# Performance work log

Measured on AMD Instinct MI355X. Metric: run time of the kernel, lower is better.

## Reference

```python
import jax, jax.numpy as jnp
import numpy as np

D_MODEL = 1024
N_HEADS = 16
ADAPTIVE_TEMP = 1.0
LN_EPS = 1e-5


def _sinusoidal_pe(max_len, d_model):
    pos = np.arange(max_len)[:, None].astype(np.float32)
    div = np.exp(np.arange(0, d_model, 2).astype(np.float32) * (-np.log(10000.0) / d_model))
    pe = np.zeros((max_len, d_model), dtype=np.float32)
    pe[:, 0::2] = np.sin(pos * div)
    pe[:, 1::2] = np.cos(pos * div)
    return jnp.asarray(pe)


def _mlp2(q, w1, b1, w2, b2):
    # Linear(1,h) -> ReLU -> Linear(h,d)
    return jax.nn.relu(q @ w1 + b1) @ w2 + b2


def setup_inputs() -> dict:
    key = jax.random.key(0)
    ks = jax.random.split(key, 24)
    B, T, D = 2, 2048, D_MODEL
    H2 = D // 2
    s = 0.02
    inp = {
        "x": jax.random.normal(ks[0], (B, T, D), jnp.float32),
        "quantile": jax.random.uniform(ks[1], (B, 1), jnp.float32),
        "quantile_importance": jax.random.uniform(ks[2], (100,), jnp.float32),
        "Wq": jax.random.normal(ks[3], (D, D), jnp.float32) * s,
        "bq": jnp.zeros((D,), jnp.float32),
        "Wk": jax.random.normal(ks[4], (D, D), jnp.float32) * s,
        "bk": jnp.zeros((D,), jnp.float32),
        "Wv": jax.random.normal(ks[5], (D, D), jnp.float32) * s,
        "bv": jnp.zeros((D,), jnp.float32),
        "Wo": jax.random.normal(ks[6], (D, D), jnp.float32) * s,
        "bo": jnp.zeros((D,), jnp.float32),
        "qpq_w1": jax.random.normal(ks[7], (1, H2), jnp.float32) * s,
        "qpq_b1": jnp.zeros((H2,), jnp.float32),
        "qpq_w2": jax.random.normal(ks[8], (H2, D), jnp.float32) * s,
        "qpq_b2": jnp.zeros((D,), jnp.float32),
        "qpk_w1": jax.random.normal(ks[9], (1, H2), jnp.float32) * s,
        "qpk_b1": jnp.zeros((H2,), jnp.float32),
        "qpk_w2": jax.random.normal(ks[10], (H2, D), jnp.float32) * s,
        "qpk_b2": jnp.zeros((D,), jnp.float32),
        "qpv_w1": jax.random.normal(ks[11], (1, H2), jnp.float32) * s,
        "qpv_b1": jnp.zeros((H2,), jnp.float32),
        "qpv_w2": jax.random.normal(ks[12], (H2, D), jnp.float32) * s,
        "qpv_b2": jnp.zeros((D,), jnp.float32),
        "ln_g": jnp.ones((D,), jnp.float32),
        "ln_b": jnp.zeros((D,), jnp.float32),
    }
    return inp


def reference(x, quantile, quantile_importance,
              Wq, bq, Wk, bk, Wv, bv, Wo, bo,
              qpq_w1, qpq_b1, qpq_w2, qpq_b2,
              qpk_w1, qpk_b1, qpk_w2, qpk_b2,
              qpv_w1, qpv_b1, qpv_w2, qpv_b2,
              ln_g, ln_b):
    B, T, D = x.shape
    H = N_HEADS
    dk = D // H

    # positional encoding
    x = x + _sinusoidal_pe(T, D)

    # quantile-conditioned embeddings [B, D]
    q_embed = _mlp2(quantile, qpq_w1, qpq_b1, qpq_w2, qpq_b2)
    k_embed = _mlp2(quantile, qpk_w1, qpk_b1, qpk_w2, qpk_b2)
    v_embed = _mlp2(quantile, qpv_w1, qpv_b1, qpv_w2, qpv_b2)

    # importance weight per batch (no-grad buffer lookup)
    buf = jax.lax.stop_gradient(quantile_importance)
    idx = jnp.clip((quantile[:, 0] * 100).astype(jnp.int32), 0, 99)
    mx = buf.max()
    imp = buf[idx]
    imp = jnp.where(mx > 0, imp / mx, imp)  # [B]

    Q = (x @ Wq + bq) + q_embed[:, None, :]
    K = (x @ Wk + bk) + k_embed[:, None, :]
    V = (x @ Wv + bv) + v_embed[:, None, :]

    # [B, H, T, dk]
    Q = Q.reshape(B, T, H, dk).transpose(0, 2, 1, 3)
    K = K.reshape(B, T, H, dk).transpose(0, 2, 1, 3)
    V = V.reshape(B, T, H, dk).transpose(0, 2, 1, 3)

    scores = jnp.einsum('bhtd,bhsd->bhts', Q, K) / jnp.sqrt(jnp.float32(dk))
    scale = 1.0 + imp * ADAPTIVE_TEMP  # [B]
    scores = scores * scale[:, None, None, None]

    attn = jax.nn.softmax(scores, axis=-1)  # dropout is identity at inference
    out = jnp.einsum('bhts,bhsd->bhtd', attn, V)
    out = out.transpose(0, 2, 1, 3).reshape(B, T, D)
    out = out @ Wo + bo

    y = x + out
    mu = y.mean(axis=-1, keepdims=True)
    var = y.var(axis=-1, keepdims=True)
    return (y - mu) / jnp.sqrt(var + LN_EPS) * ln_g + ln_b
```

## Files before the change

kernel.cpp:

```cpp
#include <hip/hip_runtime.h>

#define D 1024
#define T 2048
#define BATCH 2
#define NR 4096
#define NH 16
#define HID 512

typedef unsigned short u16;
typedef unsigned int u32;
typedef unsigned long long u64;
typedef float f32x4 __attribute__((ext_vector_type(4)));
typedef float f32x16 __attribute__((ext_vector_type(16)));
typedef __bf16 bf16x8 __attribute__((ext_vector_type(8)));

__device__ __forceinline__ u16 f2bf(float f) {
    union { __bf16 h; u16 u; } c; c.h = (__bf16)f; return c.u;
}

__device__ __forceinline__ u32 cvtpk(float a, float b) {
    u32 r;
    asm("v_cvt_pk_bf16_f32 %0, %1, %2" : "=v"(r) : "v"(a), "v"(b));
    return r;
}

__device__ __forceinline__ void plswap(u32& x, u32& y) {
    asm volatile("v_permlane32_swap_b32 %0, %1" : "+v"(x), "+v"(y));
}

__device__ __forceinline__ float fmax3(float a, float b, float c) {
    float r; asm("v_max3_f32 %0, %1, %2, %3" : "=v"(r) : "v"(a), "v"(b), "v"(c)); return r;
}

__device__ __forceinline__ float vmax16(const f32x16& v) {
    float c0 = fmax3(v[0], v[1], v[2]);
    float c1 = fmax3(v[3], v[4], v[5]);
    float c2 = fmax3(v[6], v[7], v[8]);
    float c3 = fmax3(v[9], v[10], v[11]);
    c0 = fmax3(c0, v[12], v[13]);
    c1 = fmax3(c1, v[14], v[15]);
    c0 = fmax3(c0, c1, c2);
    return fmaxf(c0, c3);
}

__device__ __forceinline__ void gload16(const u16* g, u16* l) {
    __builtin_amdgcn_global_load_lds(
        (const __attribute__((address_space(1))) unsigned int*)g,
        (__attribute__((address_space(3))) unsigned int*)l,
        16, 0, 0);
}

__device__ __forceinline__ int swz8(int row) {
    return (row & 7) ^ ((row >> 3) & 3);
}

__global__ __launch_bounds__(256) void k_mlp1(const float* __restrict__ qtl,
        const float* __restrict__ w1q, const float* __restrict__ b1q, const float* __restrict__ w2q,
        const float* __restrict__ w1k, const float* __restrict__ b1k, const float* __restrict__ w2k,
        const float* __restrict__ w1v, const float* __restrict__ b1v, const float* __restrict__ w2v,
        const float* __restrict__ qimp, float* __restrict__ part, float* __restrict__ scl)
{
    int dc = blockIdx.x;
    int jc = blockIdx.y;
    int wb = blockIdx.z;
    int which = wb >> 1, b = wb & 1;
    const float *w1, *b1, *w2;
    if (which == 0)      { w1 = w1q; b1 = b1q; w2 = w2q; }
    else if (which == 1) { w1 = w1k; b1 = b1k; w2 = w2k; }
    else                 { w1 = w1v; b1 = b1v; w2 = w2v; }
    int tid = threadIdx.x;
    __shared__ float h[128];
    if (tid < 128) {
        int j = jc * 128 + tid;
        h[tid] = fmaxf(qtl[b] * w1[j] + b1[j], 0.0f);
    }
    __syncthreads();
    int d = dc * 256 + tid;
    float acc = 0.0f;
    for (int j = 0; j < 128; ++j) acc += h[j] * w2[(size_t)(jc * 128 + j) * D + d];
    part[((size_t)wb * 4 + jc) * D + d] = acc;
    if (dc == 0 && jc == 0 && wb == 0 && tid < BATCH) {
        float mx = qimp[0];
        for (int i = 1; i < 100; ++i) mx = fmaxf(mx, qimp[i]);
        float q = qtl[tid];
        int idx = (int)(q * 100.0f);
        idx = idx < 0 ? 0 : (idx > 99 ? 99 : idx);
        float imp = qimp[idx];
        if (mx > 0.0f) imp /= mx;
        scl[tid] = 1.0f + imp;
    }
}

__global__ __launch_bounds__(256) void k_mlp2(const float* __restrict__ part,
        const float* __restrict__ b2q, const float* __restrict__ b2k, const float* __restrict__ b2v,
        float* __restrict__ embeds)
{
    int dc = blockIdx.x;
    int wb = blockIdx.y;
    int which = wb >> 1;
    const float* b2 = which == 0 ? b2q : which == 1 ? b2k : b2v;
    int d = dc * 256 + threadIdx.x;
    float acc = b2[d];
    #pragma unroll
    for (int jc = 0; jc < 4; ++jc) acc += part[((size_t)wb * 4 + jc) * D + d];
    embeds[(size_t)wb * D + d] = acc;
}

__global__ __launch_bounds__(256) void k_prep(const float* __restrict__ x,
                                              float* __restrict__ xpe, u16* __restrict__ xpeb,
                                              const float* __restrict__ Wq, const float* __restrict__ Wk,
                                              const float* __restrict__ Wv, const float* __restrict__ Wo,
                                              u16* __restrict__ Wt)
{
    if (blockIdx.x < 4096) {
        int idx = (blockIdx.x * 256 + threadIdx.x) * 4;
        int d = idx & (D - 1);
        int t = (idx >> 10) & (T - 1);
        const float KL = -0.0089944731946f;
        float ft = (float)t;
        float dv0 = __expf((float)d * KL);
        float dv1 = __expf((float)(d + 2) * KL);
        float a0 = ft * dv0, a1 = ft * dv1;
        float4 xv = *reinterpret_cast<const float4*>(x + idx);
        float4 r;
        r.x = xv.x + __sinf(a0);
        r.y = xv.y + __cosf(a0);
        r.z = xv.z + __sinf(a1);
        r.w = xv.w + __cosf(a1);
        *reinterpret_cast<float4*>(xpe + idx) = r;
        ushort4 o;
        o.x = f2bf(r.x); o.y = f2bf(r.y); o.z = f2bf(r.z); o.w = f2bf(r.w);
        *reinterpret_cast<ushort4*>(xpeb + idx) = o;
        return;
    }
    __shared__ float tile[64][65];
    int bi = blockIdx.x - 4096;
    int z = bi >> 8;
    const float* W = z == 0 ? Wq : z == 1 ? Wk : z == 2 ? Wv : Wo;
    u16* out = Wt + (size_t)z * D * D;
    int n0 = (bi & 15) * 64, k0 = ((bi >> 4) & 15) * 64;
    int r = threadIdx.x >> 4;
    int c4 = (threadIdx.x & 15) * 4;
    #pragma unroll
    for (int rr = 0; rr < 64; rr += 16) {
        float4 v = *reinterpret_cast<const float4*>(W + (size_t)(k0 + r + rr) * D + n0 + c4);
        tile[r + rr][c4 + 0] = v.x; tile[r + rr][c4 + 1] = v.y;
        tile[r + rr][c4 + 2] = v.z; tile[r + rr][c4 + 3] = v.w;
    }
    __syncthreads();
    #pragma unroll
    for (int rr = 0; rr < 64; rr += 16) {
        ushort4 o;
        o.x = f2bf(tile[c4 + 0][r + rr]);
        o.y = f2bf(tile[c4 + 1][r + rr]);
        o.z = f2bf(tile[c4 + 2][r + rr]);
        o.w = f2bf(tile[c4 + 3][r + rr]);
        *reinterpret_cast<ushort4*>(out + (size_t)(n0 + r + rr) * D + k0 + c4) = o;
    }
}

__device__ __forceinline__ void gemm128(const u16* __restrict__ Ag, const u16* __restrict__ Bg,
                                        int m0, int n0, f32x4 acc[4][4])
{
    __shared__ u16 As[2][128 * 64];
    __shared__ u16 Bs[2][128 * 64];
    const int tid = threadIdx.x;
    const int lane = tid & 63, wave = tid >> 6;
    const int wr = wave >> 1, wc = wave & 1;
    #pragma unroll
    for (int i = 0; i < 4; ++i)
        #pragma unroll
        for (int j = 0; j < 4; ++j)
            #pragma unroll
            for (int e = 0; e < 4; ++e) acc[i][j][e] = 0.0f;

    #pragma unroll
    for (int c = 0; c < 4; ++c) {
        int ci = c * 256 + tid;
        int row = ci >> 3;
        int sl = (ci & 7) ^ (row & 7);
        gload16(Ag + (size_t)(m0 + row) * D + sl * 8, As[0] + (size_t)ci * 8);
        gload16(Bg + (size_t)(n0 + row) * D + sl * 8, Bs[0] + (size_t)ci * 8);
    }
    __syncthreads();

    for (int kt = 0; kt < 16; ++kt) {
        int cur = kt & 1;
        if (kt < 15) {
            int k0 = (kt + 1) * 64;
            #pragma unroll
            for (int c = 0; c < 4; ++c) {
                int ci = c * 256 + tid;
                int row = ci >> 3;
                int sl = (ci & 7) ^ (row & 7);
                gload16(Ag + (size_t)(m0 + row) * D + k0 + sl * 8, As[cur ^ 1] + (size_t)ci * 8);
                gload16(Bg + (size_t)(n0 + row) * D + k0 + sl * 8, Bs[cur ^ 1] + (size_t)ci * 8);
            }
        }
        #pragma unroll
        for (int ks = 0; ks < 2; ++ks) {
            bf16x8 af[4], bfr[4];
            #pragma unroll
            for (int i = 0; i < 4; ++i) {
                int ra = wr * 64 + i * 16 + (lane & 15);
                int sa = ((ks * 4 + (lane >> 4)) ^ (ra & 7));
                af[i] = *reinterpret_cast<const bf16x8*>((const char*)As[cur] + ra * 128 + sa * 16);
                int rb = wc * 64 + i * 16 + (lane & 15);
                int sb = ((ks * 4 + (lane >> 4)) ^ (rb & 7));
                bfr[i] = *reinterpret_cast<const bf16x8*>((const char*)Bs[cur] + rb * 128 + sb * 16);
            }
            #pragma unroll
            for (int i = 0; i < 4; ++i)
                #pragma unroll
                for (int j = 0; j < 4; ++j)
                    acc[i][j] = __builtin_amdgcn_mfma_f32_16x16x32_bf16(af[i], bfr[j], acc[i][j], 0, 0, 0);
        }
        __syncthreads();
    }
}

__global__ __launch_bounds__(256, 2)
void k_qkv(const u16* __restrict__ A, const u16* __restrict__ Wt,
           const float* __restrict__ bq, const float* __restrict__ bk, const float* __restrict__ bv,
           const float* __restrict__ embeds, const float* __restrict__ scl,
           u16* __restrict__ Qo, u16* __restrict__ Ko, u16* __restrict__ Vt)
{
    int which = blockIdx.z;
    const u16* Bg = Wt + (size_t)which * D * D;
    const float* bias = which == 0 ? bq : which == 1 ? bk : bv;
    const float* emb = embeds + which * (BATCH * D);
    int m0 = blockIdx.x * 128, n0 = blockIdx.y * 128;
    f32x4 acc[4][4];
    gemm128(A, Bg, m0, n0, acc);
    int lane = threadIdx.x & 63, wave = threadIdx.x >> 6;
    int wr = wave >> 1, wc = wave & 1;
    int rowbase = m0 + wr * 64 + ((lane >> 4) << 2);
    int colbase = n0 + wc * 64 + (lane & 15);
    if (which < 2) {
        u16* Out = which == 0 ? Qo : Ko;
        float sc0 = 1.0f, sc1 = 1.0f;
        if (which == 0) {
            sc0 = scl[0] * 0.125f * 1.44269504f;
            sc1 = scl[1] * 0.125f * 1.44269504f;
        }
        #pragma unroll
        for (int j = 0; j < 4; ++j) {
            int c = colbase + j * 16;
            float add0 = bias[c] + emb[c];
            float add1 = bias[c] + emb[D + c];
            #pragma unroll
            for (int i = 0; i < 4; ++i) {
                int rb = rowbase + i * 16;
                #pragma unroll
                for (int jj = 0; jj < 4; ++jj) {
                    int r = rb + jj;
                    float v = (r >> 11) ? (acc[i][j][jj] + add1) * sc1
                                        : (acc[i][j][jj] + add0) * sc0;
                    Out[(size_t)r * D + c] = f2bf(v);
                }
            }
        }
    } else {
        #pragma unroll
        for (int j = 0; j < 4; ++j) {
            int c = colbase + j * 16;
            int hh = c >> 6, cc = c & 63;
            float add0 = bias[c] + emb[c];
            float add1 = bias[c] + emb[D + c];
            #pragma unroll
            for (int i = 0; i < 4; ++i) {
                int rb = rowbase + i * 16;
                int bb = rb >> 11;
                int t = rb & (T - 1);
                float add = bb ? add1 : add0;
                ushort4 o;
                o.x = f2bf(acc[i][j][0] + add);
                o.y = f2bf(acc[i][j][1] + add);
                o.z = f2bf(acc[i][j][2] + add);
                o.w = f2bf(acc[i][j][3] + add);
                *reinterpret_cast<ushort4*>(Vt + ((size_t)((bb * NH + hh) * 64 + cc)) * T + t) = o;
            }
        }
    }
}

__global__ __launch_bounds__(512, 4)
void k_attn(const u16* __restrict__ Q, const u16* __restrict__ K, const u16* __restrict__ Vt,
            u16* __restrict__ AO)
{
    __shared__ u16 Ks[2][2][64 * 64];
    __shared__ u16 Vs[2][2][64 * 64];
    int bh = blockIdx.x;
    int b = bh >> 4, hh = bh & 15;
    int q0 = blockIdx.y * 128;
    int tid = threadIdx.x;
    int lane = tid & 63, w = tid >> 6;
    int half = w >> 2, wq = w & 3;
    int q31 = lane & 31, h = lane >> 5;
    int sh = tid >> 8, sti = tid & 255;
    int kvb = sh * 1024;

    bf16x8 qf[4];
    {
        const u16* qp = Q + (size_t)(b * T + q0 + wq * 32 + q31) * D + hh * 64 + h * 8;
        #pragma unroll
        for (int ds = 0; ds < 4; ++ds)
            qf[ds] = *reinterpret_cast<const bf16x8*>(qp + ds * 16);
    }

    f32x16 o0, o1;
    #pragma unroll
    for (int e = 0; e < 16; ++e) { o0[e] = 0.0f; o1[e] = 0.0f; }
    float m_run = -1e30f, l_run = 0.0f;

    #pragma unroll
    for (int c = 0; c < 2; ++c) {
        int ci = c * 256 + sti;
        int row = ci >> 3;
        int sl = (ci & 7) ^ swz8(row);
        gload16(K + (size_t)(b * T + kvb + row) * D + hh * 64 + sl * 8, Ks[sh][0] + (size_t)ci * 8);
        gload16(Vt + (size_t)(bh * 64 + row) * T + kvb + sl * 8, Vs[sh][0] + (size_t)ci * 8);
    }
    __syncthreads();

    for (int kt = 0; kt < 16; ++kt) {
        int cur = kt & 1;
        if (kt < 15) {
            int t0 = kvb + (kt + 1) * 64;
            #pragma unroll
            for (int c = 0; c < 2; ++c) {
                int ci = c * 256 + sti;
                int row = ci >> 3;
                int sl = (ci & 7) ^ swz8(row);
                gload16(K + (size_t)(b * T + t0 + row) * D + hh * 64 + sl * 8, Ks[sh][cur ^ 1] + (size_t)ci * 8);
                gload16(Vt + (size_t)(bh * 64 + row) * T + t0 + sl * 8, Vs[sh][cur ^ 1] + (size_t)ci * 8);
            }
        }
        const char* Ksc = (const char*)Ks[half][cur];
        const char* Vsc = (const char*)Vs[half][cur];

        f32x16 s[2];
        #pragma unroll
        for (int k2 = 0; k2 < 2; ++k2)
            #pragma unroll
            for (int e = 0; e < 16; ++e) s[k2][e] = 0.0f;
        __builtin_amdgcn_s_setprio(1);
        #pragma unroll
        for (int k2 = 0; k2 < 2; ++k2) {
            int rk = k2 * 32 + q31;
            int xm = swz8(rk);
            #pragma unroll
            for (int ds = 0; ds < 4; ++ds) {
                int sp = (2 * ds + h) ^ xm;
                bf16x8 kf = *reinterpret_cast<const bf16x8*>(Ksc + rk * 128 + sp * 16);
                s[k2] = __builtin_amdgcn_mfma_f32_32x32x16_bf16(kf, qf[ds], s[k2], 0, 0, 0);
            }
        }
        __builtin_amdgcn_s_setprio(0);

        float mt = fmaxf(vmax16(s[0]), vmax16(s[1]));
        mt = fmaxf(mt, __shfl_xor(mt, 32, 64));
        bool skip = __all((int)(mt <= m_run + 11.0f));
        if (!skip) {
            float mn = fmaxf(m_run, mt);
            float corr = __builtin_exp2f(m_run - mn);
            m_run = mn;
            l_run *= corr;
            #pragma unroll
            for (int reg = 0; reg < 16; ++reg) {
                int src = ((reg & 3) + 8 * (reg >> 2)) + ((lane & 32) >> 3);
                float cr = __shfl(corr, src, 64);
                o0[reg] *= cr;
                o1[reg] *= cr;
            }
        }
        float ps0 = 0.0f, ps1 = 0.0f, ps2 = 0.0f, ps3 = 0.0f;
        #pragma unroll
        for (int k2 = 0; k2 < 2; ++k2)
            #pragma unroll
            for (int e = 0; e < 16; ++e) {
                float p = __builtin_exp2f(s[k2][e] - m_run);
                s[k2][e] = p;
                if ((e & 3) == 0) ps0 += p; else if ((e & 3) == 1) ps1 += p;
                else if ((e & 3) == 2) ps2 += p; else ps3 += p;
            }
        float psum = (ps0 + ps1) + (ps2 + ps3);
        psum += __shfl_xor(psum, 32, 64);
        l_run += psum;

        __builtin_amdgcn_s_setprio(1);
        #pragma unroll
        for (int k2 = 0; k2 < 2; ++k2) {
            u32 w0 = cvtpk(s[k2][0], s[k2][1]),   w1 = cvtpk(s[k2][2], s[k2][3]);
            u32 w2 = cvtpk(s[k2][4], s[k2][5]),   w3 = cvtpk(s[k2][6], s[k2][7]);
            u32 w4 = cvtpk(s[k2][8], s[k2][9]),   w5 = cvtpk(s[k2][10], s[k2][11]);
            u32 w6 = cvtpk(s[k2][12], s[k2][13]), w7 = cvtpk(s[k2][14], s[k2][15]);
            plswap(w0, w2); plswap(w1, w3);
            plswap(w4, w6); plswap(w5, w7);
            union { bf16x8 v; u32 u[4]; } plo, phi;
            plo.u[0] = w0; plo.u[1] = w1; plo.u[2] = w2; plo.u[3] = w3;
            phi.u[0] = w4; phi.u[1] = w5; phi.u[2] = w6; phi.u[3] = w7;
            int rv0 = q31, rv1 = 32 + q31;
            int x0 = swz8(rv0), x1 = swz8(rv1);
            int klo = 2 * k2, khi = 2 * k2 + 1;
            bf16x8 vf;
            vf = *reinterpret_cast<const bf16x8*>(Vsc + rv0 * 128 + (((2 * klo + h) ^ x0) << 4));
            o0 = __builtin_amdgcn_mfma_f32_32x32x16_bf16(plo.v, vf, o0, 0, 0, 0);
            vf = *reinterpret_cast<const bf16x8*>(Vsc + rv1 * 128 + (((2 * klo + h) ^ x1) << 4));
            o1 = __builtin_amdgcn_mfma_f32_32x32x16_bf16(plo.v, vf, o1, 0, 0, 0);
            vf = *reinterpret_cast<const bf16x8*>(Vsc + rv0 * 128 + (((2 * khi + h) ^ x0) << 4));
            o0 = __builtin_amdgcn_mfma_f32_32x32x16_bf16(phi.v, vf, o0, 0, 0, 0);
            vf = *reinterpret_cast<const bf16x8*>(Vsc + rv1 * 128 + (((2 * khi + h) ^ x1) << 4));
            o1 = __builtin_amdgcn_mfma_f32_32x32x16_bf16(phi.v, vf, o1, 0, 0, 0);
        }
        __builtin_amdgcn_s_setprio(0);
        __syncthreads();
    }

    float* ML = (float*)Ks;
    float* OB = (float*)Vs;
    if (half == 1) {
        if (h == 0) {
            ML[(wq * 2 + 0) * 32 + q31] = m_run;
            ML[(wq * 2 + 1) * 32 + q31] = l_run;
        }
        #pragma unroll
        for (int reg = 0; reg < 16; ++reg) {
            int row = (reg & 3) + 8 * (reg >> 2) + 4 * h;
            OB[((size_t)wq * 32 + row) * 64 + q31] = o0[reg];
            OB[((size_t)wq * 32 + row) * 64 + 32 + q31] = o1[reg];
        }
    }
    __syncthreads();
    if (half == 0) {
        float mB = ML[(wq * 2 + 0) * 32 + q31];
        float lB = ML[(wq * 2 + 1) * 32 + q31];
        float mn = fmaxf(m_run, mB);
        float ca = __builtin_exp2f(m_run - mn);
        float cb = __builtin_exp2f(mB - mn);
        float lf = ca * l_run + cb * lB;
        float fa = ca / lf, fb = cb / lf;
        #pragma unroll
        for (int reg = 0; reg < 16; ++reg) {
            int src = ((reg & 3) + 8 * (reg >> 2)) + ((lane & 32) >> 3);
            float far = __shfl(fa, src, 64);
            float fbr = __shfl(fb, src, 64);
            int row = (reg & 3) + 8 * (reg >> 2) + 4 * h;
            float b0 = OB[((size_t)wq * 32 + row) * 64 + q31];
            float b1 = OB[((size_t)wq * 32 + row) * 64 + 32 + q31];
            int qr = q0 + wq * 32 + row;
            size_t off = (size_t)(b * T + qr) * D + hh * 64 + q31;
            AO[off] = f2bf(o0[reg] * far + b0 * fbr);
            AO[off + 32] = f2bf(o1[reg] * far + b1 * fbr);
        }
    }
}

__global__ __launch_bounds__(256, 2)
void k_ogemm(const u16* __restrict__ A, const u16* __restrict__ Wt,
             const float* __restrict__ bo, const float* __restrict__ xpe,
             float* __restrict__ y)
{
    int m0 = blockIdx.x * 128, n0 = blockIdx.y * 128;
    f32x4 acc[4][4];
    gemm128(A, Wt, m0, n0, acc);
    int lane = threadIdx.x & 63, wave = threadIdx.x >> 6;
    int wr = wave >> 1, wc = wave & 1;
    int rowbase = m0 + wr * 64 + ((lane >> 4) << 2);
    int colbase = n0 + wc * 64 + (lane & 15);
    #pragma unroll
    for (int j = 0; j < 4; ++j) {
        int c = colbase + j * 16;
        float bc = bo[c];
        #pragma unroll
        for (int i = 0; i < 4; ++i) {
            #pragma unroll
            for (int jj = 0; jj < 4; ++jj) {
                int r = rowbase + i * 16 + jj;
                y[(size_t)r * D + c] = acc[i][j][jj] + bc + xpe[(size_t)r * D + c];
            }
        }
    }
}

__global__ __launch_bounds__(256) void k_ln(const float* __restrict__ y, const float* __restrict__ g,
                                            const float* __restrict__ bb, float* __restrict__ out)
{
    int row = blockIdx.x;
    int tid = threadIdx.x;
    const float* yr = y + (size_t)row * D;
    float4 v = *reinterpret_cast<const float4*>(yr + tid * 4);
    float s = v.x + v.y + v.z + v.w;
    float s2 = v.x * v.x + v.y * v.y + v.z * v.z + v.w * v.w;
    #pragma unroll
    for (int off = 1; off < 64; off <<= 1) {
        s += __shfl_xor(s, off, 64);
        s2 += __shfl_xor(s2, off, 64);
    }
    __shared__ float red[8];
    int wave = tid >> 6, lane = tid & 63;
    if (lane == 0) { red[wave] = s; red[4 + wave] = s2; }
    __syncthreads();
    s = red[0] + red[1] + red[2] + red[3];
    s2 = red[4] + red[5] + red[6] + red[7];
    float mu = s * (1.0f / 1024.0f);
    float var = s2 * (1.0f / 1024.0f) - mu * mu;
    float rstd = rsqrtf(var + 1e-5f);
    float4 gv = *reinterpret_cast<const float4*>(g + tid * 4);
    float4 bv = *reinterpret_cast<const float4*>(bb + tid * 4);
    float4 o;
    o.x = (v.x - mu) * rstd * gv.x + bv.x;
    o.y = (v.y - mu) * rstd * gv.y + bv.y;
    o.z = (v.z - mu) * rstd * gv.z + bv.z;
    o.w = (v.w - mu) * rstd * gv.w + bv.w;
    *reinterpret_cast<float4*>(out + (size_t)row * D + tid * 4) = o;
}

extern "C" void kernel_launch(void* const* d_in, const int* in_sizes, int n_in,
                              void* d_out, int out_size, void* d_ws, size_t ws_size,
                              hipStream_t stream)
{
    const float* x    = (const float*)d_in[0];
    const float* qtl  = (const float*)d_in[1];
    const float* qimp = (const float*)d_in[2];
    const float* Wq = (const float*)d_in[3];
    const float* bq = (const float*)d_in[4];
    const float* Wk = (const float*)d_in[5];
    const float* bk = (const float*)d_in[6];
    const float* Wv = (const float*)d_in[7];
    const float* bv = (const float*)d_in[8];
    const float* Wo = (const float*)d_in[9];
    const float* bo = (const float*)d_in[10];
    const float* qpq_w1 = (const float*)d_in[11];
    const float* qpq_b1 = (const float*)d_in[12];
    const float* qpq_w2 = (const float*)d_in[13];
    const float* qpq_b2 = (const float*)d_in[14];
    const float* qpk_w1 = (const float*)d_in[15];
    const float* qpk_b1 = (const float*)d_in[16];
    const float* qpk_w2 = (const float*)d_in[17];
    const float* qpk_b2 = (const float*)d_in[18];
    const float* qpv_w1 = (const float*)d_in[19];
    const float* qpv_b1 = (const float*)d_in[20];
    const float* qpv_w2 = (const float*)d_in[21];
    const float* qpv_b2 = (const float*)d_in[22];
    const float* ln_g = (const float*)d_in[23];
    const float* ln_b = (const float*)d_in[24];
    (void)in_sizes; (void)n_in; (void)out_size; (void)ws_size;

    char* w = (char*)d_ws;
    float* xpe   = (float*)(w);
    u16* xpeb    = (u16*)(w + (16u << 20));
    u16* Wt      = (u16*)(w + (24u << 20));
    u16* Qb      = (u16*)(w + (32u << 20));
    u16* Kb      = (u16*)(w + (40u << 20));
    u16* Vtb     = (u16*)(w + (48u << 20));
    u16* AOb     = (u16*)(w + (56u << 20));
    float* yb    = (float*)(w + (32u << 20));
    float* emb   = (float*)(w + (64u << 20));
    float* scl   = (float*)(w + (64u << 20) + 32768);
    float* part  = (float*)(w + (64u << 20) + 65536);

    k_mlp1<<<dim3(4, 4, 6), 256, 0, stream>>>(qtl,
        qpq_w1, qpq_b1, qpq_w2,
        qpk_w1, qpk_b1, qpk_w2,
        qpv_w1, qpv_b1, qpv_w2,
        qimp, part, scl);
    k_mlp2<<<dim3(4, 6), 256, 0, stream>>>(part, qpq_b2, qpk_b2, qpv_b2, emb);
    k_prep<<<5120, 256, 0, stream>>>(x, xpe, xpeb, Wq, Wk, Wv, Wo, Wt);
    k_qkv<<<dim3(32, 8, 3), 256, 0, stream>>>(xpeb, Wt, bq, bk, bv, emb, scl, Qb, Kb, Vtb);
    k_attn<<<dim3(32, 16), 512, 0, stream>>>(Qb, Kb, Vtb, AOb);
    k_ogemm<<<dim3(32, 8), 256, 0, stream>>>(AOb, Wt + (size_t)3 * D * D, bo, xpe, yb);
    k_ln<<<4096, 256, 0, stream>>>(yb, ln_g, ln_b, (float*)d_out);
}
```

Baseline: 167.0 us.

## Switch GEMM to 32x32x16 MFMA and single-buffer LDS tiles

Replaces the 16x16x32 bf16 MFMA tiling in the shared GEMM with 32x32x16 MFMA over a 2x2 accumulator grid per wave, rewriting the QKV and output-projection epilogues for the new register layout. The aim is fewer LDS fragment loads per MFMA and higher matrix throughput. LDS double buffering is removed in favour of a single buffer with a barrier before and after each tile load. This halves LDS use but leaves global-load latency no longer overlapped with compute.

```diff
diff --git a/kernel.cpp b/kernel.cpp
--- a/kernel.cpp
+++ b/kernel.cpp
@@ -160,62 +160,50 @@
 }
 
 __device__ __forceinline__ void gemm128(const u16* __restrict__ Ag, const u16* __restrict__ Bg,
-                                        int m0, int n0, f32x4 acc[4][4])
-{
-    __shared__ u16 As[2][128 * 64];
-    __shared__ u16 Bs[2][128 * 64];
+                                        int m0, int n0, f32x16 acc[2][2])
+{
+    __shared__ u16 As[128 * 64];
+    __shared__ u16 Bs[128 * 64];
     const int tid = threadIdx.x;
     const int lane = tid & 63, wave = tid >> 6;
     const int wr = wave >> 1, wc = wave & 1;
-    #pragma unroll
-    for (int i = 0; i < 4; ++i)
-        #pragma unroll
-        for (int j = 0; j < 4; ++j)
-            #pragma unroll
-            for (int e = 0; e < 4; ++e) acc[i][j][e] = 0.0f;
-
-    #pragma unroll
-    for (int c = 0; c < 4; ++c) {
-        int ci = c * 256 + tid;
-        int row = ci >> 3;
-        int sl = (ci & 7) ^ (row & 7);
-        gload16(Ag + (size_t)(m0 + row) * D + sl * 8, As[0] + (size_t)ci * 8);
-        gload16(Bg + (size_t)(n0 + row) * D + sl * 8, Bs[0] + (size_t)ci * 8);
-    }
-    __syncthreads();
+    const int l31 = lane & 31, hb = lane >> 5;
+    #pragma unroll
+    for (int mi = 0; mi < 2; ++mi)
+        #pragma unroll
+        for (int ni = 0; ni < 2; ++ni)
+            #pragma unroll
+            for (int e = 0; e < 16; ++e) acc[mi][ni][e] = 0.0f;
 
     for (int kt = 0; kt < 16; ++kt) {
-        int cur = kt & 1;
-        if (kt < 15) {
-            int k0 = (kt + 1) * 64;
-            #pragma unroll
-            for (int c = 0; c < 4; ++c) {
-                int ci = c * 256 + tid;
-                int row = ci >> 3;
-                int sl = (ci & 7) ^ (row & 7);
-                gload16(Ag + (size_t)(m0 + row) * D + k0 + sl * 8, As[cur ^ 1] + (size_t)ci * 8);
-                gload16(Bg + (size_t)(n0 + row) * D + k0 + sl * 8, Bs[cur ^ 1] + (size_t)ci * 8);
-            }
-        }
-        #pragma unroll
-        for (int ks = 0; ks < 2; ++ks) {
-            bf16x8 af[4], bfr[4];
-            #pragma unroll
-            for (int i = 0; i < 4; ++i) {
-                int ra = wr * 64 + i * 16 + (lane & 15);
-                int sa = ((ks * 4 + (lane >> 4)) ^ (ra & 7));
-                af[i] = *reinterpret_cast<const bf16x8*>((const char*)As[cur] + ra * 128 + sa * 16);
-                int rb = wc * 64 + i * 16 + (lane & 15);
-                int sb = ((ks * 4 + (lane >> 4)) ^ (rb & 7));
-                bfr[i] = *reinterpret_cast<const bf16x8*>((const char*)Bs[cur] + rb * 128 + sb * 16);
-            }
-            #pragma unroll
-            for (int i = 0; i < 4; ++i)
+        __syncthreads();
+        #pragma unroll
+        for (int c = 0; c < 4; ++c) {
+            int ci = c * 256 + tid;
+            int row = ci >> 3;
+            int sl = (ci & 7) ^ swz8(row);
+            gload16(Ag + (size_t)(m0 + row) * D + kt * 64 + sl * 8, As + (size_t)ci * 8);
+            gload16(Bg + (size_t)(n0 + row) * D + kt * 64 + sl * 8, Bs + (size_t)ci * 8);
+        }
+        __syncthreads();
+        #pragma unroll
+        for (int ks = 0; ks < 4; ++ks) {
+            bf16x8 af[2], bfr[2];
+            #pragma unroll
+            for (int mi = 0; mi < 2; ++mi) {
+                int ra = wr * 64 + mi * 32 + l31;
+                int sa = (2 * ks + hb) ^ swz8(ra);
+                af[mi] = *reinterpret_cast<const bf16x8*>((const char*)As + ra * 128 + sa * 16);
+                int rb = wc * 64 + mi * 32 + l31;
+                int sb = (2 * ks + hb) ^ swz8(rb);
+                bfr[mi] = *reinterpret_cast<const bf16x8*>((const char*)Bs + rb * 128 + sb * 16);
+            }
+            #pragma unroll
+            for (int mi = 0; mi < 2; ++mi)
                 #pragma unroll
-                for (int j = 0; j < 4; ++j)
-                    acc[i][j] = __builtin_amdgcn_mfma_f32_16x16x32_bf16(af[i], bfr[j], acc[i][j], 0, 0, 0);
-        }
-        __syncthreads();
+                for (int ni = 0; ni < 2; ++ni)
+                    acc[mi][ni] = __builtin_amdgcn_mfma_f32_32x32x16_bf16(af[mi], bfr[ni], acc[mi][ni], 0, 0, 0);
+        }
     }
 }
 
@@ -230,12 +218,11 @@
     const float* bias = which == 0 ? bq : which == 1 ? bk : bv;
     const float* emb = embeds + which * (BATCH * D);
     int m0 = blockIdx.x * 128, n0 = blockIdx.y * 128;
-    f32x4 acc[4][4];
+    f32x16 acc[2][2];
     gemm128(A, Bg, m0, n0, acc);
     int lane = threadIdx.x & 63, wave = threadIdx.x >> 6;
     int wr = wave >> 1, wc = wave & 1;
-    int rowbase = m0 + wr * 64 + ((lane >> 4) << 2);
-    int colbase = n0 + wc * 64 + (lane & 15);
+    int l31 = lane & 31, hb = lane >> 5;
     if (which < 2) {
         u16* Out = which == 0 ? Qo : Ko;
         float sc0 = 1.0f, sc1 = 1.0f;
@@ -244,41 +231,43 @@
             sc1 = scl[1] * 0.125f * 1.44269504f;
         }
         #pragma unroll
-        for (int j = 0; j < 4; ++j) {
-            int c = colbase + j * 16;
+        for (int ni = 0; ni < 2; ++ni) {
+            int c = n0 + wc * 64 + ni * 32 + l31;
             float add0 = bias[c] + emb[c];
             float add1 = bias[c] + emb[D + c];
             #pragma unroll
-            for (int i = 0; i < 4; ++i) {
-                int rb = rowbase + i * 16;
+            for (int mi = 0; mi < 2; ++mi) {
                 #pragma unroll
-                for (int jj = 0; jj < 4; ++jj) {
-                    int r = rb + jj;
-                    float v = (r >> 11) ? (acc[i][j][jj] + add1) * sc1
-                                        : (acc[i][j][jj] + add0) * sc0;
+                for (int reg = 0; reg < 16; ++reg) {
+                    int r = m0 + wr * 64 + mi * 32 + (reg & 3) + 8 * (reg >> 2) + 4 * hb;
+                    float v = (r >> 11) ? (acc[mi][ni][reg] + add1) * sc1
+                                        : (acc[mi][ni][reg] + add0) * sc0;
                     Out[(size_t)r * D + c] = f2bf(v);
                 }
             }
         }
     } else {
         #pragma unroll
-        for (int j = 0; j < 4; ++j) {
-            int c = colbase + j * 16;
+        for (int ni = 0; ni < 2; ++ni) {
+            int c = n0 + wc * 64 + ni * 32 + l31;
             int hh = c >> 6, cc = c & 63;
             float add0 = bias[c] + emb[c];
             float add1 = bias[c] + emb[D + c];
             #pragma unroll
-            for (int i = 0; i < 4; ++i) {
-                int rb = rowbase + i * 16;
-                int bb = rb >> 11;
-                int t = rb & (T - 1);
-                float add = bb ? add1 : add0;
-                ushort4 o;
-                o.x = f2bf(acc[i][j][0] + add);
-                o.y = f2bf(acc[i][j][1] + add);
-                o.z = f2bf(acc[i][j][2] + add);
-                o.w = f2bf(acc[i][j][3] + add);
-                *reinterpret_cast<ushort4*>(Vt + ((size_t)((bb * NH + hh) * 64 + cc)) * T + t) = o;
+            for (int mi = 0; mi < 2; ++mi) {
+                #pragma unroll
+                for (int g2 = 0; g2 < 4; ++g2) {
+                    int r = m0 + wr * 64 + mi * 32 + 8 * g2 + 4 * hb;
+                    int bb = r >> 11;
+                    int t = r & (T - 1);
+                    float add = bb ? add1 : add0;
+                    ushort4 o;
+                    o.x = f2bf(acc[mi][ni][4 * g2 + 0] + add);
+                    o.y = f2bf(acc[mi][ni][4 * g2 + 1] + add);
+                    o.z = f2bf(acc[mi][ni][4 * g2 + 2] + add);
+                    o.w = f2bf(acc[mi][ni][4 * g2 + 3] + add);
+                    *reinterpret_cast<ushort4*>(Vt + ((size_t)((bb * NH + hh) * 64 + cc)) * T + t) = o;
+                }
             }
         }
     }
@@ -462,22 +451,21 @@
              float* __restrict__ y)
 {
     int m0 = blockIdx.x * 128, n0 = blockIdx.y * 128;
-    f32x4 acc[4][4];
+    f32x16 acc[2][2];
     gemm128(A, Wt, m0, n0, acc);
     int lane = threadIdx.x & 63, wave = threadIdx.x >> 6;
     int wr = wave >> 1, wc = wave & 1;
-    int rowbase = m0 + wr * 64 + ((lane >> 4) << 2);
-    int colbase = n0 + wc * 64 + (lane & 15);
-    #pragma unroll
-    for (int j = 0; j < 4; ++j) {
-        int c = colbase + j * 16;
+    int l31 = lane & 31, hb = lane >> 5;
+    #pragma unroll
+    for (int ni = 0; ni < 2; ++ni) {
+        int c = n0 + wc * 64 + ni * 32 + l31;
         float bc = bo[c];
         #pragma unroll
-        for (int i = 0; i < 4; ++i) {
-            #pragma unroll
-            for (int jj = 0; jj < 4; ++jj) {
-                int r = rowbase + i * 16 + jj;
-                y[(size_t)r * D + c] = acc[i][j][jj] + bc + xpe[(size_t)r * D + c];
+        for (int mi = 0; mi < 2; ++mi) {
+            #pragma unroll
+            for (int reg = 0; reg < 16; ++reg) {
+                int r = m0 + wr * 64 + mi * 32 + (reg & 3) + 8 * (reg >> 2) + 4 * hb;
+                y[(size_t)r * D + c] = acc[mi][ni][reg] + bc + xpe[(size_t)r * D + c];
             }
         }
     }
```

After: 149.0 us (median of 2 runs). 1.12x faster.
